# Optimization experiments

Measured on AMD Instinct MI355X. Metric: run time of the kernel, lower is better.

The kernel has to match this reference:

```python
import jax, jax.numpy as jnp
import numpy as np

K = 7          # kernel_size
PAD = K // 2   # padding = 3
G = 16         # groups = channels // group_channels = 256 // 16
GC = 16        # group_channels
EPS = 1e-5     # BatchNorm eps


def setup_inputs() -> dict:
    key = jax.random.key(0)
    ks = jax.random.split(key, 8)
    B, C, H, W = 4, 256, 56, 56
    Cr = C // 4  # reduction_ratio = 4
    x = jax.random.normal(ks[0], (B, C, H, W), dtype=jnp.float32)
    W_reduce = jax.random.normal(ks[1], (Cr, C), dtype=jnp.float32) * 0.05
    b_reduce = jax.random.normal(ks[2], (Cr,), dtype=jnp.float32) * 0.01
    bn_gamma = jnp.ones((Cr,), dtype=jnp.float32)
    bn_beta = jnp.zeros((Cr,), dtype=jnp.float32)
    bn_mean = jax.random.normal(ks[3], (Cr,), dtype=jnp.float32) * 0.01
    bn_var = jax.random.uniform(ks[4], (Cr,), dtype=jnp.float32, minval=0.5, maxval=1.5)
    W_span = jax.random.normal(ks[5], (K * K * G, Cr), dtype=jnp.float32) * 0.05
    b_span = jax.random.normal(ks[6], (K * K * G,), dtype=jnp.float32) * 0.01
    return {
        "x": x,
        "W_reduce": W_reduce, "b_reduce": b_reduce,
        "bn_gamma": bn_gamma, "bn_beta": bn_beta,
        "bn_mean": bn_mean, "bn_var": bn_var,
        "W_span": W_span, "b_span": b_span,
    }


def _involution(x, W_reduce, b_reduce, bn_gamma, bn_beta, bn_mean, bn_var, W_span, b_span):
    B, C, H, W = x.shape
    # --- kernel generation path (stride=1 -> initial_mapping is Identity) ---
    # 1x1 conv reduce: [B, Cr, H, W]
    xr = jnp.einsum('oc,bchw->bohw', W_reduce, x) + b_reduce[None, :, None, None]
    # BatchNorm (eval mode, running stats) + ReLU
    inv_std = jax.lax.rsqrt(bn_var + EPS)
    xr = (xr - bn_mean[None, :, None, None]) * (bn_gamma * inv_std)[None, :, None, None] \
         + bn_beta[None, :, None, None]
    xr = jax.nn.relu(xr)
    # 1x1 conv span: [B, K*K*G, H, W] -> [B, G, K^2, H*W]
    kern = jnp.einsum('oc,bchw->bohw', W_span, xr) + b_span[None, :, None, None]
    kern = kern.reshape(B, G, K * K, H * W)
    # --- unfold: sliding K x K windows, torch ordering (c, kh, kw) ---
    xp = jnp.pad(x, ((0, 0), (0, 0), (PAD, PAD), (PAD, PAD)))
    # [B, C, K^2, H, W]; fixed 49-iteration loop over kernel offsets
    patches = jnp.stack(
        [xp[:, :, i:i + H, j:j + W] for i in range(K) for j in range(K)], axis=2)
    patches = patches.reshape(B, G, GC, K * K, H * W)
    # multiply dynamic kernels (broadcast over group_channels) and reduce over K^2
    out = jnp.einsum('bgkl,bgckl->bgcl', kern, patches)
    return out.reshape(B, C, H, W)


def reference(x, W_reduce, b_reduce, bn_gamma, bn_beta, bn_mean, bn_var, W_span, b_span):
    return _involution(x, W_reduce, b_reduce, bn_gamma, bn_beta,
                       bn_mean, bn_var, W_span, b_span)
```

## Files before the change

### kernel.cpp

```cpp
#include <hip/hip_runtime.h>
#include <hip/hip_bf16.h>

#define HW    3136
#define C_IN  256
#define G_    16
#define GC_   16
#define IMGH  56
#define IMGW  56
#define EPSV  1e-5f

#define PROWS 62
#define XROW  64
#define SXCH  528
#define SKROW 2940

typedef __bf16 bf16x8 __attribute__((ext_vector_type(8)));
typedef float  f32x4  __attribute__((ext_vector_type(4)));

static __device__ __forceinline__ unsigned short f2bf(float f) {
    union { float f; unsigned u; } v; v.f = f;
    unsigned r = (v.u + 0x7FFFu + ((v.u >> 16) & 1u)) >> 16;
    return (unsigned short)r;
}
static __device__ __forceinline__ float bf2f(unsigned short s) {
    union { unsigned u; float f; } v; v.u = (unsigned)s << 16;
    return v.f;
}

__global__ __launch_bounds__(256) void k_prep(
    const float* __restrict__ x, const float* __restrict__ Wr,
    const float* __restrict__ Wspan, unsigned short* __restrict__ xpad,
    unsigned short* __restrict__ Wbf, unsigned short* __restrict__ Wsbf)
{
    int blk = blockIdx.x, t = threadIdx.x;
    if (blk < 496) {
        int F0 = blk * 1024 + t;
#pragma unroll
        for (int it = 0; it < 4; ++it) {
            int F   = F0 + it * 256;
            int bc  = F / 496;
            int rem = F - bc * 496;
            int row = rem >> 3, oct = rem & 7;
            int hr  = row - 3;
            const float* xs = x + (size_t)bc * HW + hr * IMGW;
            union { unsigned short s[8]; uint4 v; } pk;
#pragma unroll
            for (int j = 0; j < 8; ++j) {
                int wc = oct * 8 + j - 3;
                float vv = (hr >= 0 && hr < IMGH && wc >= 0 && wc < IMGW) ? xs[wc] : 0.f;
                pk.s[j] = f2bf(vv);
            }
            *(uint4*)(xpad + ((size_t)bc * PROWS + row) * XROW + oct * 8) = pk.v;
        }
    } else {
        int i4 = ((blk - 496) * 256 + t) * 4;
        if (i4 < 16384) {
#pragma unroll
            for (int j = 0; j < 4; ++j) Wbf[i4 + j] = f2bf(Wr[i4 + j]);
        } else {
            int j0 = i4 - 16384;
#pragma unroll
            for (int j = 0; j < 4; ++j) Wsbf[j0 + j] = f2bf(Wspan[j0 + j]);
        }
    }
}

__global__ __launch_bounds__(128) void k_reduce(
    const float* __restrict__ x,  const unsigned short* __restrict__ Wbf,
    const float* __restrict__ br, const float* __restrict__ gamma,
    const float* __restrict__ beta, const float* __restrict__ mean,
    const float* __restrict__ var, unsigned short* __restrict__ xrT)
{
    int t = threadIdx.x, wv = t >> 6, lane = t & 63;
    int ln = lane & 15, quad = lane >> 4;
    int p = blockIdx.x * 32 + wv * 16 + ln;
    int b = blockIdx.x / 98;
    int l = p - b * HW;
    const float* xb = x + (size_t)b * C_IN * HW + l;

    f32x4 acc[4];
#pragma unroll
    for (int mt = 0; mt < 4; ++mt) acc[mt] = (f32x4){0.f, 0.f, 0.f, 0.f};

#pragma unroll
    for (int ks = 0; ks < 8; ++ks) {
        int c0 = ks * 32 + quad * 8;
        float xv[8];
#pragma unroll
        for (int j = 0; j < 8; ++j) xv[j] = xb[(size_t)(c0 + j) * HW];
        union { unsigned short s[8]; bf16x8 v; } bfx;
#pragma unroll
        for (int j = 0; j < 8; ++j) bfx.s[j] = f2bf(xv[j]);
#pragma unroll
        for (int mt = 0; mt < 4; ++mt) {
            bf16x8 af = *(const bf16x8*)(Wbf + (size_t)(mt * 16 + ln) * C_IN + c0);
            acc[mt] = __builtin_amdgcn_mfma_f32_16x16x32_bf16(af, bfx.v, acc[mt], 0, 0, 0);
        }
    }
#pragma unroll
    for (int mt = 0; mt < 4; ++mt) {
        union { unsigned short s[4]; uint2 v; } pk;
#pragma unroll
        for (int r = 0; r < 4; ++r) {
            int o = mt * 16 + quad * 4 + r;
            float s  = gamma[o] * rsqrtf(var[o] + EPSV);
            float vv = (acc[mt][r] + br[o] - mean[o]) * s + beta[o];
            pk.s[r] = f2bf(fmaxf(vv, 0.f));
        }
        *(uint2*)(xrT + (size_t)p * 64 + mt * 16 + quad * 4) = pk.v;
    }
}

__global__ __launch_bounds__(512, 6) void k_invol(
    const unsigned short* __restrict__ xpad, const unsigned short* __restrict__ xrT,
    const unsigned short* __restrict__ Wsbf, const float* __restrict__ bspan,
    float* __restrict__ out)
{
    __shared__ __align__(16) unsigned short s_x[GC_ * SXCH];
    __shared__ __align__(16) float s_kern[2 * SKROW];

    int t = threadIdx.x;
    int bid = blockIdx.x;
    int xcd = bid & 7, jj = bid >> 3;
    int g = jj & 15, rpb = jj >> 4;
    int idx = xcd * 14 + rpb;
    int b = idx / 28, rp = idx - b * 28;
    int h0 = rp * 2;

    int wv = t >> 6, lane = t & 63;

#pragma unroll
    for (int i = 0; i < 2; ++i) {
        int c = wv * 2 + i;
        const unsigned short* gsrc = xpad
            + ((size_t)(b * C_IN + g * GC_ + c) * PROWS + h0) * XROW + lane * 8;
        __builtin_amdgcn_global_load_lds(
            (const __attribute__((address_space(1))) void*)gsrc,
            (__attribute__((address_space(3))) void*)&s_x[c * SXCH],
            16, 0, 0);
    }

    {
        int ln = lane & 15, quad = lane >> 4;
        int mt = wv & 3, nh = wv >> 2;
        int m0 = mt * 16;
        int ko_a = m0 + ln; if (ko_a > 48) ko_a = 48;
        const unsigned short* wrow = Wsbf + (size_t)(g * 49 + ko_a) * 64;
        int pixbase = b * HW + h0 * IMGW;

        f32x4 acc[4];
#pragma unroll
        for (int nt = 0; nt < 4; ++nt) acc[nt] = (f32x4){0.f, 0.f, 0.f, 0.f};

#pragma unroll
        for (int ks = 0; ks < 2; ++ks) {
            int c0 = ks * 32 + quad * 8;
            bf16x8 af = *(const bf16x8*)(wrow + c0);
#pragma unroll
            for (int nt = 0; nt < 4; ++nt) {
                int pp = nh * 64 + nt * 16 + ln;
                if (pp > 111) pp = 111;
                bf16x8 bb = *(const bf16x8*)(xrT + (size_t)(pixbase + pp) * 64 + c0);
                acc[nt] = __builtin_amdgcn_mfma_f32_16x16x32_bf16(af, bb, acc[nt], 0, 0, 0);
            }
        }
#pragma unroll
        for (int r = 0; r < 4; ++r) {
            int ko = m0 + quad * 4 + r;
            float bias = bspan[g * 49 + (ko < 49 ? ko : 48)];
#pragma unroll
            for (int nt = 0; nt < 4; ++nt) {
                int pp = nh * 64 + nt * 16 + ln;
                if (ko < 49 && pp < 112) {
                    int prow = pp / 56, pw = pp - prow * 56;
                    s_kern[prow * SKROW + ko * 60 + pw] = acc[nt][r] + bias;
                }
            }
        }
    }
    __syncthreads();

    if (t < 224) {
        int wp  = t % 14;
        int row = (t / 14) & 1;
        int cp  = t / 28;
        int w0  = wp * 4, c0 = cp * 2;

        const float* sk = s_kern + row * SKROW + w0;
        float a0[4], a1[4];
#pragma unroll
        for (int j = 0; j < 4; ++j) { a0[j] = 0.f; a1[j] = 0.f; }

#pragma unroll
        for (int r = 0; r < 7; ++r) {
            float4 kv[7];
#pragma unroll
            for (int dw = 0; dw < 7; ++dw)
                kv[dw] = *(const float4*)(sk + (r * 7 + dw) * 60);
#pragma unroll
            for (int ci = 0; ci < 2; ++ci) {
                const unsigned short* sx = s_x + (c0 + ci) * SXCH + (row + r) * XROW + w0;
                union { unsigned short s[12]; uint2 v[3]; } xr_;
                xr_.v[0] = *(const uint2*)(sx);
                xr_.v[1] = *(const uint2*)(sx + 4);
                xr_.v[2] = *(const uint2*)(sx + 8);
                float xf[10];
#pragma unroll
                for (int j = 0; j < 10; ++j) xf[j] = bf2f(xr_.s[j]);
                float* aa = ci ? a1 : a0;
#pragma unroll
                for (int dw = 0; dw < 7; ++dw) {
                    aa[0] += kv[dw].x * xf[dw];
                    aa[1] += kv[dw].y * xf[dw + 1];
                    aa[2] += kv[dw].z * xf[dw + 2];
                    aa[3] += kv[dw].w * xf[dw + 3];
                }
            }
        }
        float* ob = out + (size_t)(b * C_IN + g * GC_ + c0) * HW + (h0 + row) * IMGW + w0;
        *(float4*)ob = make_float4(a0[0], a0[1], a0[2], a0[3]);
        *(float4*)(ob + HW) = make_float4(a1[0], a1[1], a1[2], a1[3]);
    }
}

extern "C" void kernel_launch(void* const* d_in, const int* in_sizes, int n_in,
                              void* d_out, int out_size, void* d_ws, size_t ws_size,
                              hipStream_t stream)
{
    const float* x   = (const float*)d_in[0];
    const float* Wr  = (const float*)d_in[1];
    const float* br  = (const float*)d_in[2];
    const float* gm  = (const float*)d_in[3];
    const float* bt  = (const float*)d_in[4];
    const float* mn  = (const float*)d_in[5];
    const float* vr  = (const float*)d_in[6];
    const float* Ws  = (const float*)d_in[7];
    const float* bs  = (const float*)d_in[8];
    float* out = (float*)d_out;

    char* ws = (char*)d_ws;
    unsigned short* xrT  = (unsigned short*)ws;
    unsigned short* xpad = (unsigned short*)(ws + 1605632);
    unsigned short* Wbf  = (unsigned short*)(ws + 9732096);
    unsigned short* Wsbf = (unsigned short*)(ws + 9764864);

    k_prep  <<<dim3(561),  256, 0, stream>>>(x, Wr, Ws, xpad, Wbf, Wsbf);
    k_reduce<<<dim3(392),  128, 0, stream>>>(x, Wbf, br, gm, bt, mn, vr, xrT);
    k_invol <<<dim3(1792), 512, 0, stream>>>(xpad, xrT, Wsbf, bs, out);
}
```

Measured before the change: 116.2 us.

## Transpose x to pixel-major bf16 in prep and split reduce GEMM over output halves

The prep kernel gains extra blocks that transpose x through shared memory into a pixel-major bf16 buffer (xT). The reduce kernel then reads contiguous 16-byte channel vectors per pixel instead of strided fp32 loads across channels. Reduce blocks are reorganized to 256 threads, each covering 64 pixels and half of the 64 output channels. This trades an extra 6.4MB write plus re-read for coalesced, better-parallelized reduce loads.

```diff
diff --git a/kernel.cpp b/kernel.cpp
--- a/kernel.cpp
+++ b/kernel.cpp
@@ -30,8 +30,10 @@
 __global__ __launch_bounds__(256) void k_prep(
     const float* __restrict__ x, const float* __restrict__ Wr,
     const float* __restrict__ Wspan, unsigned short* __restrict__ xpad,
-    unsigned short* __restrict__ Wbf, unsigned short* __restrict__ Wsbf)
-{
+    unsigned short* __restrict__ Wbf, unsigned short* __restrict__ Wsbf,
+    unsigned short* __restrict__ xT)
+{
+    __shared__ float s_t[64][65];
     int blk = blockIdx.x, t = threadIdx.x;
     if (blk < 496) {
         int F0 = blk * 1024 + t;
@@ -52,7 +54,7 @@
             }
             *(uint4*)(xpad + ((size_t)bc * PROWS + row) * XROW + oct * 8) = pk.v;
         }
-    } else {
+    } else if (blk < 561) {
         int i4 = ((blk - 496) * 256 + t) * 4;
         if (i4 < 16384) {
 #pragma unroll
@@ -62,52 +64,71 @@
 #pragma unroll
             for (int j = 0; j < 4; ++j) Wsbf[j0 + j] = f2bf(Wspan[j0 + j]);
         }
-    }
-}
-
-__global__ __launch_bounds__(128) void k_reduce(
-    const float* __restrict__ x,  const unsigned short* __restrict__ Wbf,
+    } else {
+        int q  = blk - 561;
+        int pb = q % 49, cb = (q / 49) & 3, b = q / 196;
+        int P0 = pb * 64, C0 = cb * 64;
+        int c = t >> 2, jq = t & 3;
+        const float* xs = x + (size_t)(b * C_IN + C0 + c) * HW + P0 + jq * 16;
+#pragma unroll
+        for (int k = 0; k < 4; ++k) {
+            float4 v = *(const float4*)(xs + k * 4);
+            s_t[c][jq * 16 + k * 4 + 0] = v.x;
+            s_t[c][jq * 16 + k * 4 + 1] = v.y;
+            s_t[c][jq * 16 + k * 4 + 2] = v.z;
+            s_t[c][jq * 16 + k * 4 + 3] = v.w;
+        }
+        __syncthreads();
+        int pix = t & 63, cq = t >> 6;
+        union { unsigned short s[16]; uint4 v[2]; } pk;
+#pragma unroll
+        for (int k = 0; k < 16; ++k)
+            pk.s[k] = f2bf(s_t[cq * 16 + k][pix]);
+        unsigned short* dst = xT + ((size_t)b * HW + P0 + pix) * 256 + C0 + cq * 16;
+        *(uint4*)dst       = pk.v[0];
+        *(uint4*)(dst + 8) = pk.v[1];
+    }
+}
+
+__global__ __launch_bounds__(256) void k_reduce(
+    const unsigned short* __restrict__ xT, const unsigned short* __restrict__ Wbf,
     const float* __restrict__ br, const float* __restrict__ gamma,
     const float* __restrict__ beta, const float* __restrict__ mean,
     const float* __restrict__ var, unsigned short* __restrict__ xrT)
 {
     int t = threadIdx.x, wv = t >> 6, lane = t & 63;
     int ln = lane & 15, quad = lane >> 4;
-    int p = blockIdx.x * 32 + wv * 16 + ln;
-    int b = blockIdx.x / 98;
-    int l = p - b * HW;
-    const float* xb = x + (size_t)b * C_IN * HW + l;
-
-    f32x4 acc[4];
-#pragma unroll
-    for (int mt = 0; mt < 4; ++mt) acc[mt] = (f32x4){0.f, 0.f, 0.f, 0.f};
+    int bi = blockIdx.x;
+    int mh = bi / 196;
+    int p  = (bi % 196) * 64 + wv * 16 + ln;
+
+    const unsigned short* xrow = xT + (size_t)p * 256;
+
+    f32x4 acc[2];
+    acc[0] = (f32x4){0.f, 0.f, 0.f, 0.f};
+    acc[1] = (f32x4){0.f, 0.f, 0.f, 0.f};
 
 #pragma unroll
     for (int ks = 0; ks < 8; ++ks) {
         int c0 = ks * 32 + quad * 8;
-        float xv[8];
-#pragma unroll
-        for (int j = 0; j < 8; ++j) xv[j] = xb[(size_t)(c0 + j) * HW];
-        union { unsigned short s[8]; bf16x8 v; } bfx;
-#pragma unroll
-        for (int j = 0; j < 8; ++j) bfx.s[j] = f2bf(xv[j]);
-#pragma unroll
-        for (int mt = 0; mt < 4; ++mt) {
-            bf16x8 af = *(const bf16x8*)(Wbf + (size_t)(mt * 16 + ln) * C_IN + c0);
-            acc[mt] = __builtin_amdgcn_mfma_f32_16x16x32_bf16(af, bfx.v, acc[mt], 0, 0, 0);
-        }
-    }
-#pragma unroll
-    for (int mt = 0; mt < 4; ++mt) {
+        bf16x8 bb = *(const bf16x8*)(xrow + c0);
+#pragma unroll
+        for (int mt = 0; mt < 2; ++mt) {
+            bf16x8 af = *(const bf16x8*)(Wbf + (size_t)(mh * 32 + mt * 16 + ln) * C_IN + c0);
+            acc[mt] = __builtin_amdgcn_mfma_f32_16x16x32_bf16(af, bb, acc[mt], 0, 0, 0);
+        }
+    }
+#pragma unroll
+    for (int mt = 0; mt < 2; ++mt) {
         union { unsigned short s[4]; uint2 v; } pk;
 #pragma unroll
         for (int r = 0; r < 4; ++r) {
-            int o = mt * 16 + quad * 4 + r;
+            int o = mh * 32 + mt * 16 + quad * 4 + r;
             float s  = gamma[o] * rsqrtf(var[o] + EPSV);
             float vv = (acc[mt][r] + br[o] - mean[o]) * s + beta[o];
             pk.s[r] = f2bf(fmaxf(vv, 0.f));
         }
-        *(uint2*)(xrT + (size_t)p * 64 + mt * 16 + quad * 4) = pk.v;
+        *(uint2*)(xrT + (size_t)p * 64 + mh * 32 + mt * 16 + quad * 4) = pk.v;
     }
 }
 
@@ -243,8 +264,9 @@
     unsigned short* xpad = (unsigned short*)(ws + 1605632);
     unsigned short* Wbf  = (unsigned short*)(ws + 9732096);
     unsigned short* Wsbf = (unsigned short*)(ws + 9764864);
-
-    k_prep  <<<dim3(561),  256, 0, stream>>>(x, Wr, Ws, xpad, Wbf, Wsbf);
-    k_reduce<<<dim3(392),  128, 0, stream>>>(x, Wbf, br, gm, bt, mn, vr, xrT);
+    unsigned short* xT   = (unsigned short*)(ws + 9865216);
+
+    k_prep  <<<dim3(1345), 256, 0, stream>>>(x, Wr, Ws, xpad, Wbf, Wsbf, xT);
+    k_reduce<<<dim3(392),  256, 0, stream>>>(xT, Wbf, br, gm, bt, mn, vr, xrT);
     k_invol <<<dim3(1792), 512, 0, stream>>>(xpad, xrT, Wsbf, bs, out);
 }
```

After: 123.0 us. 5.9% more time.

## Merge prep and reduce kernels; widen involution per-thread tile with packed FMA

Applied to the files above, without the earlier changes.

Folds the bf16 conversion and the 1x1 reduce GEMM into one front kernel. Each reduce block now converts W_reduce to bf16 in shared memory itself, which removes a kernel launch and the Wbf round trip through global memory. The involution inner loop gives each thread 8 output pixels instead of 4 and computes them with packed 2-wide float FMAs over 16-byte LDS loads. This halves the number of active compute threads (112 instead of 224). Launch bounds drop to 4 waves per SIMD to make room for the larger per-thread register footprint, at the cost of occupancy and parallelism.

```diff
diff --git a/kernel.cpp b/kernel.cpp
--- a/kernel.cpp
+++ b/kernel.cpp
@@ -13,26 +13,35 @@
 #define XROW  64
 #define SXCH  528
 #define SKROW 2940
+#define SWSTR 264
 
 typedef __bf16 bf16x8 __attribute__((ext_vector_type(8)));
 typedef float  f32x4  __attribute__((ext_vector_type(4)));
+typedef float  f32x2  __attribute__((ext_vector_type(2)));
 
 static __device__ __forceinline__ unsigned short f2bf(float f) {
     union { float f; unsigned u; } v; v.f = f;
     unsigned r = (v.u + 0x7FFFu + ((v.u >> 16) & 1u)) >> 16;
     return (unsigned short)r;
 }
-static __device__ __forceinline__ float bf2f(unsigned short s) {
-    union { unsigned u; float f; } v; v.u = (unsigned)s << 16;
-    return v.f;
-}
-
-__global__ __launch_bounds__(256) void k_prep(
+static __device__ __forceinline__ float bfu_lo(unsigned u) {
+    union { unsigned u; float f; } v; v.u = u << 16; return v.f;
+}
+static __device__ __forceinline__ float bfu_hi(unsigned u) {
+    union { unsigned u; float f; } v; v.u = u & 0xffff0000u; return v.f;
+}
+
+__global__ __launch_bounds__(256) void k_front(
     const float* __restrict__ x, const float* __restrict__ Wr,
-    const float* __restrict__ Wspan, unsigned short* __restrict__ xpad,
-    unsigned short* __restrict__ Wbf, unsigned short* __restrict__ Wsbf)
+    const float* __restrict__ Wspan, const float* __restrict__ br,
+    const float* __restrict__ gamma, const float* __restrict__ beta,
+    const float* __restrict__ mean, const float* __restrict__ var,
+    unsigned short* __restrict__ xpad, unsigned short* __restrict__ Wsbf,
+    unsigned short* __restrict__ xrT)
 {
+    __shared__ __align__(16) unsigned short s_w[64 * SWSTR];
     int blk = blockIdx.x, t = threadIdx.x;
+
     if (blk < 496) {
         int F0 = blk * 1024 + t;
 #pragma unroll
@@ -52,66 +61,71 @@
             }
             *(uint4*)(xpad + ((size_t)bc * PROWS + row) * XROW + oct * 8) = pk.v;
         }
+    } else if (blk < 545) {
+        int i4 = ((blk - 496) * 256 + t) * 4;
+#pragma unroll
+        for (int j = 0; j < 4; ++j) Wsbf[i4 + j] = f2bf(Wspan[i4 + j]);
     } else {
-        int i4 = ((blk - 496) * 256 + t) * 4;
-        if (i4 < 16384) {
-#pragma unroll
-            for (int j = 0; j < 4; ++j) Wbf[i4 + j] = f2bf(Wr[i4 + j]);
-        } else {
-            int j0 = i4 - 16384;
-#pragma unroll
-            for (int j = 0; j < 4; ++j) Wsbf[j0 + j] = f2bf(Wspan[j0 + j]);
-        }
-    }
-}
-
-__global__ __launch_bounds__(128) void k_reduce(
-    const float* __restrict__ x,  const unsigned short* __restrict__ Wbf,
-    const float* __restrict__ br, const float* __restrict__ gamma,
-    const float* __restrict__ beta, const float* __restrict__ mean,
-    const float* __restrict__ var, unsigned short* __restrict__ xrT)
-{
-    int t = threadIdx.x, wv = t >> 6, lane = t & 63;
-    int ln = lane & 15, quad = lane >> 4;
-    int p = blockIdx.x * 32 + wv * 16 + ln;
-    int b = blockIdx.x / 98;
-    int l = p - b * HW;
-    const float* xb = x + (size_t)b * C_IN * HW + l;
-
-    f32x4 acc[4];
-#pragma unroll
-    for (int mt = 0; mt < 4; ++mt) acc[mt] = (f32x4){0.f, 0.f, 0.f, 0.f};
-
-#pragma unroll
-    for (int ks = 0; ks < 8; ++ks) {
-        int c0 = ks * 32 + quad * 8;
-        float xv[8];
-#pragma unroll
-        for (int j = 0; j < 8; ++j) xv[j] = xb[(size_t)(c0 + j) * HW];
-        union { unsigned short s[8]; bf16x8 v; } bfx;
-#pragma unroll
-        for (int j = 0; j < 8; ++j) bfx.s[j] = f2bf(xv[j]);
+        int bi = blk - 545;
+        int wv = t >> 6, lane = t & 63;
+        int ln = lane & 15, quad = lane >> 4;
+        int p  = bi * 64 + wv * 16 + ln;
+        int b  = bi / 49;
+        int l  = p - b * HW;
+        const float* xb = x + (size_t)b * C_IN * HW + l;
+
+        float xv[64];
+#pragma unroll
+        for (int ks = 0; ks < 8; ++ks)
+#pragma unroll
+            for (int j = 0; j < 8; ++j)
+                xv[ks * 8 + j] = xb[(size_t)(ks * 32 + quad * 8 + j) * HW];
+
+        {
+            int row = t >> 2, col0 = (t & 3) * 64;
+            const float* wsrc = Wr + t * 64;
+#pragma unroll
+            for (int k = 0; k < 8; ++k) {
+                union { unsigned short s[8]; uint4 v; } pk;
+#pragma unroll
+                for (int j = 0; j < 8; ++j) pk.s[j] = f2bf(wsrc[k * 8 + j]);
+                *(uint4*)&s_w[row * SWSTR + col0 + k * 8] = pk.v;
+            }
+        }
+        __syncthreads();
+
+        f32x4 acc[4];
+#pragma unroll
+        for (int mt = 0; mt < 4; ++mt) acc[mt] = (f32x4){0.f, 0.f, 0.f, 0.f};
+
+#pragma unroll
+        for (int ks = 0; ks < 8; ++ks) {
+            union { unsigned short s[8]; bf16x8 v; } bfx;
+#pragma unroll
+            for (int j = 0; j < 8; ++j) bfx.s[j] = f2bf(xv[ks * 8 + j]);
+            int c0 = ks * 32 + quad * 8;
+#pragma unroll
+            for (int mt = 0; mt < 4; ++mt) {
+                bf16x8 af = *(const bf16x8*)&s_w[(mt * 16 + ln) * SWSTR + c0];
+                acc[mt] = __builtin_amdgcn_mfma_f32_16x16x32_bf16(af, bfx.v, acc[mt], 0, 0, 0);
+            }
+        }
 #pragma unroll
         for (int mt = 0; mt < 4; ++mt) {
-            bf16x8 af = *(const bf16x8*)(Wbf + (size_t)(mt * 16 + ln) * C_IN + c0);
-            acc[mt] = __builtin_amdgcn_mfma_f32_16x16x32_bf16(af, bfx.v, acc[mt], 0, 0, 0);
-        }
-    }
-#pragma unroll
-    for (int mt = 0; mt < 4; ++mt) {
-        union { unsigned short s[4]; uint2 v; } pk;
-#pragma unroll
-        for (int r = 0; r < 4; ++r) {
-            int o = mt * 16 + quad * 4 + r;
-            float s  = gamma[o] * rsqrtf(var[o] + EPSV);
-            float vv = (acc[mt][r] + br[o] - mean[o]) * s + beta[o];
-            pk.s[r] = f2bf(fmaxf(vv, 0.f));
-        }
-        *(uint2*)(xrT + (size_t)p * 64 + mt * 16 + quad * 4) = pk.v;
-    }
-}
-
-__global__ __launch_bounds__(512, 6) void k_invol(
+            union { unsigned short s[4]; uint2 v; } pk;
+#pragma unroll
+            for (int r = 0; r < 4; ++r) {
+                int o = mt * 16 + quad * 4 + r;
+                float s  = gamma[o] * rsqrtf(var[o] + EPSV);
+                float vv = (acc[mt][r] + br[o] - mean[o]) * s + beta[o];
+                pk.s[r] = f2bf(fmaxf(vv, 0.f));
+            }
+            *(uint2*)(xrT + (size_t)p * 64 + mt * 16 + quad * 4) = pk.v;
+        }
+    }
+}
+
+__global__ __launch_bounds__(512, 4) void k_invol(
     const unsigned short* __restrict__ xpad, const unsigned short* __restrict__ xrT,
     const unsigned short* __restrict__ Wsbf, const float* __restrict__ bspan,
     float* __restrict__ out)
@@ -180,46 +194,64 @@
     }
     __syncthreads();
 
-    if (t < 224) {
-        int wp  = t % 14;
-        int row = (t / 14) & 1;
-        int cp  = t / 28;
-        int w0  = wp * 4, c0 = cp * 2;
+    if (t < 112) {
+        int cp  = t / 14;
+        int rem = t - cp * 14;
+        int row = rem / 7, wp = rem - row * 7;
+        int w0  = wp * 8, c0 = cp * 2;
 
         const float* sk = s_kern + row * SKROW + w0;
-        float a0[4], a1[4];
-#pragma unroll
-        for (int j = 0; j < 4; ++j) { a0[j] = 0.f; a1[j] = 0.f; }
+        f32x2 acc[2][4];
+#pragma unroll
+        for (int ci = 0; ci < 2; ++ci)
+#pragma unroll
+            for (int j = 0; j < 4; ++j) acc[ci][j] = (f32x2){0.f, 0.f};
 
 #pragma unroll
         for (int r = 0; r < 7; ++r) {
-            float4 kv[7];
-#pragma unroll
-            for (int dw = 0; dw < 7; ++dw)
-                kv[dw] = *(const float4*)(sk + (r * 7 + dw) * 60);
+            float4 ka[7], kb[7];
+#pragma unroll
+            for (int dw = 0; dw < 7; ++dw) {
+                ka[dw] = *(const float4*)(sk + (r * 7 + dw) * 60);
+                kb[dw] = *(const float4*)(sk + (r * 7 + dw) * 60 + 4);
+            }
 #pragma unroll
             for (int ci = 0; ci < 2; ++ci) {
-                const unsigned short* sx = s_x + (c0 + ci) * SXCH + (row + r) * XROW + w0;
-                union { unsigned short s[12]; uint2 v[3]; } xr_;
-                xr_.v[0] = *(const uint2*)(sx);
-                xr_.v[1] = *(const uint2*)(sx + 4);
-                xr_.v[2] = *(const uint2*)(sx + 8);
-                float xf[10];
-#pragma unroll
-                for (int j = 0; j < 10; ++j) xf[j] = bf2f(xr_.s[j]);
-                float* aa = ci ? a1 : a0;
+                const unsigned short* sx =
+                    s_x + (c0 + ci) * SXCH + (row + r) * XROW + w0;
+                uint4 xu0 = *(const uint4*)sx;
+                uint4 xu1 = *(const uint4*)(sx + 8);
+                float xf[16];
+                const unsigned* xw = (const unsigned*)&xu0;
+#pragma unroll
+                for (int k = 0; k < 4; ++k) {
+                    xf[2 * k]     = bfu_lo(xw[k]);
+                    xf[2 * k + 1] = bfu_hi(xw[k]);
+                }
+                const unsigned* xw1 = (const unsigned*)&xu1;
+#pragma unroll
+                for (int k = 0; k < 4; ++k) {
+                    xf[8 + 2 * k]     = bfu_lo(xw1[k]);
+                    xf[8 + 2 * k + 1] = bfu_hi(xw1[k]);
+                }
 #pragma unroll
                 for (int dw = 0; dw < 7; ++dw) {
-                    aa[0] += kv[dw].x * xf[dw];
-                    aa[1] += kv[dw].y * xf[dw + 1];
-                    aa[2] += kv[dw].z * xf[dw + 2];
-                    aa[3] += kv[dw].w * xf[dw + 3];
-                }
-            }
-        }
-        float* ob = out + (size_t)(b * C_IN + g * GC_ + c0) * HW + (h0 + row) * IMGW + w0;
-        *(float4*)ob = make_float4(a0[0], a0[1], a0[2], a0[3]);
-        *(float4*)(ob + HW) = make_float4(a1[0], a1[1], a1[2], a1[3]);
+                    acc[ci][0] += (f32x2){ka[dw].x, ka[dw].y} * (f32x2){xf[dw],     xf[dw + 1]};
+                    acc[ci][1] += (f32x2){ka[dw].z, ka[dw].w} * (f32x2){xf[dw + 2], xf[dw + 3]};
+                    acc[ci][2] += (f32x2){kb[dw].x, kb[dw].y} * (f32x2){xf[dw + 4], xf[dw + 5]};
+                    acc[ci][3] += (f32x2){kb[dw].z, kb[dw].w} * (f32x2){xf[dw + 6], xf[dw + 7]};
+                }
+            }
+        }
+#pragma unroll
+        for (int ci = 0; ci < 2; ++ci) {
+            float* ob = out + (size_t)(b * C_IN + g * GC_ + c0 + ci) * HW
+                            + (h0 + row) * IMGW + w0;
+            *(float4*)ob       = make_float4(acc[ci][0][0], acc[ci][0][1],
+                                             acc[ci][1][0], acc[ci][1][1]);
+            *(float4*)(ob + 4) = make_float4(acc[ci][2][0], acc[ci][2][1],
+                                             acc[ci][3][0], acc[ci][3][1]);
+        }
     }
 }
 
@@ -241,10 +273,9 @@
     char* ws = (char*)d_ws;
     unsigned short* xrT  = (unsigned short*)ws;
     unsigned short* xpad = (unsigned short*)(ws + 1605632);
-    unsigned short* Wbf  = (unsigned short*)(ws + 9732096);
-    unsigned short* Wsbf = (unsigned short*)(ws + 9764864);
-
-    k_prep  <<<dim3(561),  256, 0, stream>>>(x, Wr, Ws, xpad, Wbf, Wsbf);
-    k_reduce<<<dim3(392),  128, 0, stream>>>(x, Wbf, br, gm, bt, mn, vr, xrT);
+    unsigned short* Wsbf = (unsigned short*)(ws + 9732096);
+
+    k_front <<<dim3(741),  256, 0, stream>>>(x, Wr, Ws, br, gm, bt, mn, vr,
+                                             xpad, Wsbf, xrT);
     k_invol <<<dim3(1792), 512, 0, stream>>>(xpad, xrT, Wsbf, bs, out);
 }
```

New measurement: 114.2 us. About the same (-1.7%).
